# Kernel tuning notes

Measured on AMD Instinct MI355X. Metric: run time of the kernel, lower is better.

The kernel has to match this reference:

```python
import jax, jax.numpy as jnp
import numpy as np

E = 8        # num_experts
H = 2048     # hidden_size
I = 1408     # intermediate_size
K = 2        # top_k
B, S = 1, 2048


def setup_inputs() -> dict:
    key = jax.random.key(0)
    k1, k2, k3, k4, k5 = jax.random.split(key, 5)
    hidden_states = jax.random.normal(k1, (B, S, H), dtype=jnp.float32)
    top_k_index = jax.random.randint(k2, (B, S, K), 0, E, dtype=jnp.int32)
    top_k_weights = jax.random.uniform(k3, (B, S, K), dtype=jnp.float32)
    # scaled init so activations stay O(1)
    gate_up_proj = jax.random.normal(k4, (E, 2 * I, H), dtype=jnp.float32) / np.sqrt(H)
    down_proj = jax.random.normal(k5, (E, H, I), dtype=jnp.float32) / np.sqrt(I)
    return {
        "hidden_states": hidden_states,
        "top_k_index": top_k_index,
        "top_k_weights": top_k_weights,
        "gate_up_proj": gate_up_proj,
        "down_proj": down_proj,
    }


def reference(hidden_states, top_k_index, top_k_weights, gate_up_proj, down_proj):
    orig_shape = hidden_states.shape
    x = hidden_states.reshape(-1, H)            # [T, H]
    idx = top_k_index.reshape(-1, K)            # [T, K] int32
    w = top_k_weights.reshape(-1, K)            # [T, K]
    out = jnp.zeros_like(x)
    for e in range(E):
        # combine weight for tokens routed to expert e (0 if not routed)
        we = jnp.sum(w * (idx == e).astype(w.dtype), axis=-1)   # [T]
        gu = x @ gate_up_proj[e].T                              # [T, 2I]
        gate, up = gu[:, :I], gu[:, I:]
        h = jax.nn.silu(gate) * up                              # [T, I]
        y = h @ down_proj[e].T                                  # [T, H]
        out = out + we[:, None] * y
    return out.reshape(orig_shape)
```

## Files before the change

### kernel.cpp

```cpp
#include <hip/hip_runtime.h>
#include <hip/hip_bf16.h>

#define E_ 8
#define H_ 2048
#define I_ 1408
#define S_ 2048
#define NPAIR 4096
#define MAXMT 32

typedef short bf16x8 __attribute__((ext_vector_type(8)));
typedef ushort u16x8 __attribute__((ext_vector_type(8)));
typedef float f32x4  __attribute__((ext_vector_type(4)));

__device__ inline bf16x8 pack8(float4 a, float4 b) {
    bf16x8 r;
    const float v[8] = {a.x, a.y, a.z, a.w, b.x, b.y, b.z, b.w};
#pragma unroll
    for (int j = 0; j < 8; ++j) {
        __hip_bfloat16 t = __float2bfloat16(v[j]);
        r[j] = *reinterpret_cast<short*>(&t);
    }
    return r;
}

__global__ void moe_router(const int* __restrict__ idx,
                           int* __restrict__ counts, int* __restrict__ bases,
                           int* __restrict__ tok, int* __restrict__ inv) {
    __shared__ int cnt[E_];
    __shared__ int cur[E_];
    const int tid = threadIdx.x;
    if (tid < E_) cnt[tid] = 0;
    __syncthreads();
    for (int p = tid; p < NPAIR; p += 256)
        atomicAdd(&cnt[idx[p]], 1);
    __syncthreads();
    if (tid == 0) {
        int b = 0;
        for (int e = 0; e < E_; ++e) {
            counts[e] = cnt[e];
            bases[e]  = b;
            cur[e]    = b;
            b += cnt[e];
        }
    }
    __syncthreads();
    for (int p = tid; p < NPAIR; p += 256) {
        const int e = idx[p];
        const int pos = atomicAdd(&cur[e], 1);
        tok[pos] = p >> 1;
        inv[p]   = pos;
    }
}

__global__ void convert_x(const float* __restrict__ x, ushort* __restrict__ xb) {
    const size_t i = ((size_t)blockIdx.x * 256 + threadIdx.x) * 8;
    const float4 a = *(const float4*)(x + i);
    const float4 b = *(const float4*)(x + i + 4);
    *(bf16x8*)(xb + i) = pack8(a, b);
}

__global__ __launch_bounds__(256, 2)
void moe_gemm1(const ushort* __restrict__ xb,
               const float* __restrict__ wg,
               const int* __restrict__ counts,
               const int* __restrict__ bases,
               const int* __restrict__ tok,
               ushort* __restrict__ hbuf) {
    const int e  = blockIdx.y & (E_ - 1);
    const int mt = blockIdx.y >> 3;
    const int count = counts[e];
    if (mt * 128 >= count) return;
    const int base = bases[e];
    const int n0 = blockIdx.x * 128;
    const float* wge = wg + (size_t)e * (2 * I_) * H_;

    __shared__ alignas(16) ushort sm[2][3][5120];

    const int tid  = threadIdx.x;
    const int lane = tid & 63;
    const int wid  = tid >> 6;
    const int wm = wid & 1, wn = wid >> 1;
    const int lr = lane & 15, lq = lane >> 4;

    const f32x4 vzero = {0.f, 0.f, 0.f, 0.f};
    f32x4 accg[4][4], accu[4][4];
#pragma unroll
    for (int mi = 0; mi < 4; ++mi)
#pragma unroll
        for (int ni = 0; ni < 4; ++ni) { accg[mi][ni] = vzero; accu[mi][ni] = vzero; }

    const int srow = tid >> 2;
    const int sc8  = (tid & 3) * 8;
    const int r0 = srow, r1 = srow + 64;

    const int ia0 = mt * 128 + r0, ia1 = mt * 128 + r1;
    const bool v0 = ia0 < count, v1 = ia1 < count;
    const ushort* ap0 = xb + (size_t)(v0 ? tok[base + ia0] : 0) * H_ + sc8;
    const ushort* ap1 = xb + (size_t)(v1 ? tok[base + ia1] : 0) * H_ + sc8;
    const float* gp0 = wge + (size_t)(n0 + r0) * H_ + sc8;
    const float* gp1 = wge + (size_t)(n0 + r1) * H_ + sc8;
    const float* up0 = gp0 + (size_t)I_ * H_;
    const float* up1 = gp1 + (size_t)I_ * H_;

    const uint4 z4 = {0u, 0u, 0u, 0u};
    uint4 ra0, ra1;
    float4 rg0a, rg0b, rg1a, rg1b, ru0a, ru0b, ru1a, ru1b;

    ra0 = v0 ? *(const uint4*)ap0 : z4;
    ra1 = v1 ? *(const uint4*)ap1 : z4;
    rg0a = *(const float4*)gp0; rg0b = *(const float4*)(gp0 + 4);
    rg1a = *(const float4*)gp1; rg1b = *(const float4*)(gp1 + 4);
    ru0a = *(const float4*)up0; ru0b = *(const float4*)(up0 + 4);
    ru1a = *(const float4*)up1; ru1b = *(const float4*)(up1 + 4);
    {
        ushort* As = &sm[0][0][0]; ushort* Bg = &sm[0][1][0]; ushort* Bu = &sm[0][2][0];
        *(uint4*)&As[r0 * 40 + sc8] = ra0;
        *(uint4*)&As[r1 * 40 + sc8] = ra1;
        *(bf16x8*)&Bg[r0 * 40 + sc8] = pack8(rg0a, rg0b);
        *(bf16x8*)&Bg[r1 * 40 + sc8] = pack8(rg1a, rg1b);
        *(bf16x8*)&Bu[r0 * 40 + sc8] = pack8(ru0a, ru0b);
        *(bf16x8*)&Bu[r1 * 40 + sc8] = pack8(ru1a, ru1b);
    }
    __syncthreads();

    for (int kt = 0; kt < H_ / 32; ++kt) {
        const int cur = kt & 1;
        if (kt < H_ / 32 - 1) {
            ap0 += 32; ap1 += 32; gp0 += 32; gp1 += 32; up0 += 32; up1 += 32;
            ra0 = v0 ? *(const uint4*)ap0 : z4;
            ra1 = v1 ? *(const uint4*)ap1 : z4;
            rg0a = *(const float4*)gp0; rg0b = *(const float4*)(gp0 + 4);
            rg1a = *(const float4*)gp1; rg1b = *(const float4*)(gp1 + 4);
            ru0a = *(const float4*)up0; ru0b = *(const float4*)(up0 + 4);
            ru1a = *(const float4*)up1; ru1b = *(const float4*)(up1 + 4);
        }
        const ushort* As = &sm[cur][0][0];
        const ushort* Bg = &sm[cur][1][0];
        const ushort* Bu = &sm[cur][2][0];
        bf16x8 a[4], bg[4], bu[4];
#pragma unroll
        for (int mi = 0; mi < 4; ++mi)
            a[mi] = *(const bf16x8*)&As[(wm * 64 + mi * 16 + lr) * 40 + lq * 8];
#pragma unroll
        for (int ni = 0; ni < 4; ++ni) {
            bg[ni] = *(const bf16x8*)&Bg[(wn * 64 + ni * 16 + lr) * 40 + lq * 8];
            bu[ni] = *(const bf16x8*)&Bu[(wn * 64 + ni * 16 + lr) * 40 + lq * 8];
        }
#pragma unroll
        for (int mi = 0; mi < 4; ++mi)
#pragma unroll
            for (int ni = 0; ni < 4; ++ni) {
                accg[mi][ni] = __builtin_amdgcn_mfma_f32_16x16x32_bf16(a[mi], bg[ni], accg[mi][ni], 0, 0, 0);
                accu[mi][ni] = __builtin_amdgcn_mfma_f32_16x16x32_bf16(a[mi], bu[ni], accu[mi][ni], 0, 0, 0);
            }
        if (kt < H_ / 32 - 1) {
            ushort* nA = &sm[cur ^ 1][0][0];
            ushort* nG = &sm[cur ^ 1][1][0];
            ushort* nU = &sm[cur ^ 1][2][0];
            *(uint4*)&nA[r0 * 40 + sc8] = ra0;
            *(uint4*)&nA[r1 * 40 + sc8] = ra1;
            *(bf16x8*)&nG[r0 * 40 + sc8] = pack8(rg0a, rg0b);
            *(bf16x8*)&nG[r1 * 40 + sc8] = pack8(rg1a, rg1b);
            *(bf16x8*)&nU[r0 * 40 + sc8] = pack8(ru0a, ru0b);
            *(bf16x8*)&nU[r1 * 40 + sc8] = pack8(ru1a, ru1b);
        }
        __syncthreads();
    }

    ushort* Ht = &sm[0][0][0];
#pragma unroll
    for (int mi = 0; mi < 4; ++mi)
#pragma unroll
        for (int r = 0; r < 4; ++r) {
            const int row = wm * 64 + mi * 16 + lq * 4 + r;
#pragma unroll
            for (int ni = 0; ni < 4; ++ni) {
                const int col = wn * 64 + ni * 16 + lr;
                const float g = accg[mi][ni][r];
                const float u = accu[mi][ni][r];
                const float h = (g / (1.0f + __expf(-g))) * u;
                __hip_bfloat16 hb = __float2bfloat16(h);
                Ht[row * 136 + col] = *reinterpret_cast<ushort*>(&hb);
            }
        }
    __syncthreads();
#pragma unroll
    for (int p = 0; p < 8; ++p) {
        const int slot = p * 256 + tid;
        const int row = slot >> 4;
        const int cc  = (slot & 15) * 8;
        const int gi = mt * 128 + row;
        if (gi < count)
            *(uint4*)&hbuf[(size_t)(base + gi) * I_ + n0 + cc] = *(const uint4*)&Ht[row * 136 + cc];
    }
}

__global__ __launch_bounds__(256, 2)
void moe_gemm2(const ushort* __restrict__ hbuf,
               const float* __restrict__ wd,
               const int* __restrict__ counts,
               const int* __restrict__ bases,
               ushort* __restrict__ ybuf) {
    const int e  = blockIdx.y & (E_ - 1);
    const int mt = blockIdx.y >> 3;
    const int count = counts[e];
    if (mt * 128 >= count) return;
    const int base = bases[e];
    const int n0 = blockIdx.x * 128;
    const float* wde = wd + (size_t)e * H_ * I_;

    __shared__ alignas(16) ushort sm[2][2][5120];

    const int tid  = threadIdx.x;
    const int lane = tid & 63;
    const int wid  = tid >> 6;
    const int wm = wid & 1, wn = wid >> 1;
    const int lr = lane & 15, lq = lane >> 4;

    const f32x4 vzero = {0.f, 0.f, 0.f, 0.f};
    f32x4 acc[4][4];
#pragma unroll
    for (int mi = 0; mi < 4; ++mi)
#pragma unroll
        for (int ni = 0; ni < 4; ++ni) acc[mi][ni] = vzero;

    const int srow = tid >> 2;
    const int sc8  = (tid & 3) * 8;
    const int r0 = srow, r1 = srow + 64;

    const int ia0 = mt * 128 + r0, ia1 = mt * 128 + r1;
    const bool v0 = ia0 < count, v1 = ia1 < count;
    const ushort* ap0 = hbuf + (size_t)(base + (v0 ? ia0 : 0)) * I_ + sc8;
    const ushort* ap1 = hbuf + (size_t)(base + (v1 ? ia1 : 0)) * I_ + sc8;
    const float* bp0 = wde + (size_t)(n0 + r0) * I_ + sc8;
    const float* bp1 = wde + (size_t)(n0 + r1) * I_ + sc8;

    const uint4 z4 = {0u, 0u, 0u, 0u};
    uint4 ra0, ra1;
    float4 rb0a, rb0b, rb1a, rb1b;

    ra0 = v0 ? *(const uint4*)ap0 : z4;
    ra1 = v1 ? *(const uint4*)ap1 : z4;
    rb0a = *(const float4*)bp0; rb0b = *(const float4*)(bp0 + 4);
    rb1a = *(const float4*)bp1; rb1b = *(const float4*)(bp1 + 4);
    {
        ushort* As = &sm[0][0][0]; ushort* Bs = &sm[0][1][0];
        *(uint4*)&As[r0 * 40 + sc8] = ra0;
        *(uint4*)&As[r1 * 40 + sc8] = ra1;
        *(bf16x8*)&Bs[r0 * 40 + sc8] = pack8(rb0a, rb0b);
        *(bf16x8*)&Bs[r1 * 40 + sc8] = pack8(rb1a, rb1b);
    }
    __syncthreads();

    for (int kt = 0; kt < I_ / 32; ++kt) {
        const int cur = kt & 1;
        if (kt < I_ / 32 - 1) {
            ap0 += 32; ap1 += 32; bp0 += 32; bp1 += 32;
            ra0 = v0 ? *(const uint4*)ap0 : z4;
            ra1 = v1 ? *(const uint4*)ap1 : z4;
            rb0a = *(const float4*)bp0; rb0b = *(const float4*)(bp0 + 4);
            rb1a = *(const float4*)bp1; rb1b = *(const float4*)(bp1 + 4);
        }
        const ushort* As = &sm[cur][0][0];
        const ushort* Bs = &sm[cur][1][0];
        bf16x8 a[4], b[4];
#pragma unroll
        for (int mi = 0; mi < 4; ++mi)
            a[mi] = *(const bf16x8*)&As[(wm * 64 + mi * 16 + lr) * 40 + lq * 8];
#pragma unroll
        for (int ni = 0; ni < 4; ++ni)
            b[ni] = *(const bf16x8*)&Bs[(wn * 64 + ni * 16 + lr) * 40 + lq * 8];
#pragma unroll
        for (int mi = 0; mi < 4; ++mi)
#pragma unroll
            for (int ni = 0; ni < 4; ++ni)
                acc[mi][ni] = __builtin_amdgcn_mfma_f32_16x16x32_bf16(a[mi], b[ni], acc[mi][ni], 0, 0, 0);
        if (kt < I_ / 32 - 1) {
            ushort* nA = &sm[cur ^ 1][0][0];
            ushort* nB = &sm[cur ^ 1][1][0];
            *(uint4*)&nA[r0 * 40 + sc8] = ra0;
            *(uint4*)&nA[r1 * 40 + sc8] = ra1;
            *(bf16x8*)&nB[r0 * 40 + sc8] = pack8(rb0a, rb0b);
            *(bf16x8*)&nB[r1 * 40 + sc8] = pack8(rb1a, rb1b);
        }
        __syncthreads();
    }

    ushort* Yt = &sm[0][0][0];
#pragma unroll
    for (int mi = 0; mi < 4; ++mi)
#pragma unroll
        for (int r = 0; r < 4; ++r) {
            const int row = wm * 64 + mi * 16 + lq * 4 + r;
#pragma unroll
            for (int ni = 0; ni < 4; ++ni) {
                const int col = wn * 64 + ni * 16 + lr;
                __hip_bfloat16 yb = __float2bfloat16(acc[mi][ni][r]);
                Yt[row * 136 + col] = *reinterpret_cast<ushort*>(&yb);
            }
        }
    __syncthreads();
#pragma unroll
    for (int p = 0; p < 8; ++p) {
        const int slot = p * 256 + tid;
        const int row = slot >> 4;
        const int cc  = (slot & 15) * 8;
        const int gi = mt * 128 + row;
        if (gi < count)
            *(uint4*)&ybuf[(size_t)(base + gi) * H_ + n0 + cc] = *(const uint4*)&Yt[row * 136 + cc];
    }
}

__global__ void moe_combine(const ushort* __restrict__ ybuf,
                            const int* __restrict__ inv,
                            const float* __restrict__ tkw,
                            float* __restrict__ out) {
    const int t = blockIdx.x;
    const int c8 = threadIdx.x * 8;
    const int p0 = inv[2 * t], p1 = inv[2 * t + 1];
    const float w0 = tkw[2 * t], w1 = tkw[2 * t + 1];
    const u16x8 y0 = *(const u16x8*)(ybuf + (size_t)p0 * H_ + c8);
    const u16x8 y1 = *(const u16x8*)(ybuf + (size_t)p1 * H_ + c8);
    float o[8];
#pragma unroll
    for (int j = 0; j < 8; ++j) {
        const unsigned f0 = ((unsigned)y0[j]) << 16;
        const unsigned f1 = ((unsigned)y1[j]) << 16;
        o[j] = w0 * __uint_as_float(f0) + w1 * __uint_as_float(f1);
    }
    float* dst = out + (size_t)t * H_ + c8;
    *(float4*)dst       = make_float4(o[0], o[1], o[2], o[3]);
    *(float4*)(dst + 4) = make_float4(o[4], o[5], o[6], o[7]);
}

extern "C" void kernel_launch(void* const* d_in, const int* in_sizes, int n_in,
                              void* d_out, int out_size, void* d_ws, size_t ws_size,
                              hipStream_t stream) {
    const float* x   = (const float*)d_in[0];
    const int*   tki = (const int*)d_in[1];
    const float* tkw = (const float*)d_in[2];
    const float* wg  = (const float*)d_in[3];
    const float* wd  = (const float*)d_in[4];
    float* out = (float*)d_out;

    char* p = (char*)d_ws;
    int* counts = (int*)p;  p += 32;
    int* bases  = (int*)p;  p += 32;
    int* tok    = (int*)p;  p += NPAIR * sizeof(int);
    int* inv    = (int*)p;  p += NPAIR * sizeof(int);
    ushort* xb   = (ushort*)p; p += (size_t)S_ * H_ * 2;
    ushort* hbuf = (ushort*)p; p += (size_t)NPAIR * I_ * 2;
    ushort* ybuf = (ushort*)p; p += (size_t)NPAIR * H_ * 2;

    convert_x<<<dim3((S_ * H_) / (256 * 8)), 256, 0, stream>>>(x, xb);
    moe_router<<<dim3(1), 256, 0, stream>>>(tki, counts, bases, tok, inv);
    moe_gemm1<<<dim3(I_ / 128, E_ * MAXMT), 256, 0, stream>>>(xb, wg, counts, bases, tok, hbuf);
    moe_gemm2<<<dim3(H_ / 128, E_ * MAXMT), 256, 0, stream>>>(hbuf, wd, counts, bases, ybuf);
    moe_combine<<<dim3(S_), 256, 0, stream>>>(ybuf, inv, tkw, out);
}
```

Baseline: 427.9 us.

## Pre-convert weights to tiled bf16 and stream tiles with direct-to-LDS loads

Adds a kernel that converts both fp32 weight tensors each call into bf16 laid out as contiguous 128x32 tiles. The grouped GEMMs then load A and B tiles with global_load_lds straight into shared memory, replacing in-kernel fp32 loads and conversion. This removes repeated per-block fp32 weight conversion and halves the weight bytes read inside the GEMMs. In exchange it adds a full extra pass over all weights each call (fp32 read plus bf16 write, about 138 MB of fp32 plus 69 MB of bf16) and single-buffered loads with two barriers per k-step. The old fp32 GEMM kernels are kept as a fallback for when the workspace is too small.

```diff
diff --git a/kernel.cpp b/kernel.cpp
--- a/kernel.cpp
+++ b/kernel.cpp
@@ -8,6 +8,11 @@
 #define NPAIR 4096
 #define MAXMT 32
 
+#define NT1 22
+#define KT1 64
+#define NT2 16
+#define KT2 44
+
 typedef short bf16x8 __attribute__((ext_vector_type(8)));
 typedef ushort u16x8 __attribute__((ext_vector_type(8)));
 typedef float f32x4  __attribute__((ext_vector_type(4)));
@@ -21,6 +26,13 @@
         r[j] = *reinterpret_cast<short*>(&t);
     }
     return r;
+}
+
+__device__ __forceinline__ void gload16(const ushort* g, ushort* l) {
+    __builtin_amdgcn_global_load_lds(
+        (const __attribute__((address_space(1))) void*)g,
+        (__attribute__((address_space(3))) void*)l,
+        16, 0, 0);
 }
 
 __global__ void moe_router(const int* __restrict__ idx,
@@ -59,13 +71,240 @@
     *(bf16x8*)(xb + i) = pack8(a, b);
 }
 
+__global__ __launch_bounds__(256)
+void convert_w(const float* __restrict__ wg, const float* __restrict__ wd,
+               ushort* __restrict__ wgt, ushort* __restrict__ wdt) {
+    const int b = blockIdx.x;
+    const int tid = threadIdx.x;
+    const float* src;
+    ushort* dst;
+    int rowstride;
+    if (b < E_ * NT1 * KT1) {
+        const int e = b / (NT1 * KT1), rem = b % (NT1 * KT1);
+        const int nt = rem / KT1, kt = rem % KT1;
+        src = wg + ((size_t)e * (2 * I_) + nt * 128) * H_ + kt * 32;
+        dst = wgt + (size_t)b * 4096;
+        rowstride = H_;
+    } else {
+        const int b2 = b - E_ * NT1 * KT1;
+        const int e = b2 / (NT2 * KT2), rem = b2 % (NT2 * KT2);
+        const int nt = rem / KT2, kt = rem % KT2;
+        src = wd + ((size_t)e * H_ + nt * 128) * I_ + kt * 32;
+        dst = wdt + (size_t)b2 * 4096;
+        rowstride = I_;
+    }
+#pragma unroll
+    for (int i = 0; i < 2; ++i) {
+        const int c = tid + i * 256;
+        const int row = c >> 2, col = (c & 3) * 8;
+        const float* s = src + (size_t)row * rowstride + col;
+        const float4 a = *(const float4*)s;
+        const float4 bq = *(const float4*)(s + 4);
+        *(bf16x8*)(dst + c * 8) = pack8(a, bq);
+    }
+}
+
 __global__ __launch_bounds__(256, 2)
 void moe_gemm1(const ushort* __restrict__ xb,
-               const float* __restrict__ wg,
+               const ushort* __restrict__ wgt,
                const int* __restrict__ counts,
                const int* __restrict__ bases,
                const int* __restrict__ tok,
                ushort* __restrict__ hbuf) {
+    const int e  = blockIdx.y & (E_ - 1);
+    const int mt = blockIdx.y >> 3;
+    const int count = counts[e];
+    if (mt * 128 >= count) return;
+    const int base = bases[e];
+    const int nt = blockIdx.x;
+    const int n0 = nt * 128;
+
+    __shared__ alignas(16) ushort sm[17408];
+    ushort* smA = sm;
+    ushort* smG = sm + 4096;
+    ushort* smU = sm + 8192;
+
+    const int tid  = threadIdx.x;
+    const int lane = tid & 63;
+    const int wid  = tid >> 6;
+    const int wm = wid & 1, wn = wid >> 1;
+    const int lr = lane & 15, lq = lane >> 4;
+
+    const f32x4 vzero = {0.f, 0.f, 0.f, 0.f};
+    f32x4 accg[4][4], accu[4][4];
+#pragma unroll
+    for (int mi = 0; mi < 4; ++mi)
+#pragma unroll
+        for (int ni = 0; ni < 4; ++ni) { accg[mi][ni] = vzero; accu[mi][ni] = vzero; }
+
+    const int srow = tid >> 2;
+    const int sc8  = (tid & 3) * 8;
+    const int ia0 = mt * 128 + srow, ia1 = ia0 + 64;
+    const ushort* ap0 = xb + (size_t)(ia0 < count ? tok[base + ia0] : 0) * H_ + sc8;
+    const ushort* ap1 = xb + (size_t)(ia1 < count ? tok[base + ia1] : 0) * H_ + sc8;
+    const ushort* gp  = wgt + (size_t)(e * NT1 + nt) * KT1 * 4096 + tid * 8;
+    const ushort* up  = wgt + (size_t)(e * NT1 + nt + 11) * KT1 * 4096 + tid * 8;
+    ushort* dA0 = smA + tid * 8;
+    ushort* dA1 = smA + tid * 8 + 2048;
+    ushort* dG0 = smG + tid * 8;
+    ushort* dG1 = smG + tid * 8 + 2048;
+    ushort* dU0 = smU + tid * 8;
+    ushort* dU1 = smU + tid * 8 + 2048;
+
+    for (int kt = 0; kt < KT1; ++kt) {
+        gload16(ap0, dA0);
+        gload16(ap1, dA1);
+        gload16(gp,        dG0);
+        gload16(gp + 2048, dG1);
+        gload16(up,        dU0);
+        gload16(up + 2048, dU1);
+        ap0 += 32; ap1 += 32; gp += 4096; up += 4096;
+        __syncthreads();
+
+        bf16x8 a[4], bg[4], bu[4];
+#pragma unroll
+        for (int mi = 0; mi < 4; ++mi)
+            a[mi] = *(const bf16x8*)&smA[(wm * 64 + mi * 16 + lr) * 32 + lq * 8];
+#pragma unroll
+        for (int ni = 0; ni < 4; ++ni) {
+            bg[ni] = *(const bf16x8*)&smG[(wn * 64 + ni * 16 + lr) * 32 + lq * 8];
+            bu[ni] = *(const bf16x8*)&smU[(wn * 64 + ni * 16 + lr) * 32 + lq * 8];
+        }
+#pragma unroll
+        for (int mi = 0; mi < 4; ++mi)
+#pragma unroll
+            for (int ni = 0; ni < 4; ++ni) {
+                accg[mi][ni] = __builtin_amdgcn_mfma_f32_16x16x32_bf16(a[mi], bg[ni], accg[mi][ni], 0, 0, 0);
+                accu[mi][ni] = __builtin_amdgcn_mfma_f32_16x16x32_bf16(a[mi], bu[ni], accu[mi][ni], 0, 0, 0);
+            }
+        __syncthreads();
+    }
+
+    ushort* Ht = sm;
+#pragma unroll
+    for (int mi = 0; mi < 4; ++mi)
+#pragma unroll
+        for (int r = 0; r < 4; ++r) {
+            const int row = wm * 64 + mi * 16 + lq * 4 + r;
+#pragma unroll
+            for (int ni = 0; ni < 4; ++ni) {
+                const int col = wn * 64 + ni * 16 + lr;
+                const float g = accg[mi][ni][r];
+                const float u = accu[mi][ni][r];
+                const float h = (g / (1.0f + __expf(-g))) * u;
+                __hip_bfloat16 hb = __float2bfloat16(h);
+                Ht[row * 136 + col] = *reinterpret_cast<ushort*>(&hb);
+            }
+        }
+    __syncthreads();
+#pragma unroll
+    for (int p = 0; p < 8; ++p) {
+        const int slot = p * 256 + tid;
+        const int row = slot >> 4;
+        const int cc  = (slot & 15) * 8;
+        const int gi = mt * 128 + row;
+        if (gi < count)
+            *(uint4*)&hbuf[(size_t)(base + gi) * I_ + n0 + cc] = *(const uint4*)&Ht[row * 136 + cc];
+    }
+}
+
+__global__ __launch_bounds__(256, 2)
+void moe_gemm2(const ushort* __restrict__ hbuf,
+               const ushort* __restrict__ wdt,
+               const int* __restrict__ counts,
+               const int* __restrict__ bases,
+               ushort* __restrict__ ybuf) {
+    const int e  = blockIdx.y & (E_ - 1);
+    const int mt = blockIdx.y >> 3;
+    const int count = counts[e];
+    if (mt * 128 >= count) return;
+    const int base = bases[e];
+    const int nt = blockIdx.x;
+    const int n0 = nt * 128;
+
+    __shared__ alignas(16) ushort sm[17408];
+    ushort* smA = sm;
+    ushort* smB = sm + 4096;
+
+    const int tid  = threadIdx.x;
+    const int lane = tid & 63;
+    const int wid  = tid >> 6;
+    const int wm = wid & 1, wn = wid >> 1;
+    const int lr = lane & 15, lq = lane >> 4;
+
+    const f32x4 vzero = {0.f, 0.f, 0.f, 0.f};
+    f32x4 acc[4][4];
+#pragma unroll
+    for (int mi = 0; mi < 4; ++mi)
+#pragma unroll
+        for (int ni = 0; ni < 4; ++ni) acc[mi][ni] = vzero;
+
+    const int srow = tid >> 2;
+    const int sc8  = (tid & 3) * 8;
+    const int ia0 = mt * 128 + srow, ia1 = ia0 + 64;
+    const ushort* ap0 = hbuf + (size_t)(base + (ia0 < count ? ia0 : 0)) * I_ + sc8;
+    const ushort* ap1 = hbuf + (size_t)(base + (ia1 < count ? ia1 : 0)) * I_ + sc8;
+    const ushort* bp  = wdt + (size_t)(e * NT2 + nt) * KT2 * 4096 + tid * 8;
+    ushort* dA0 = smA + tid * 8;
+    ushort* dA1 = smA + tid * 8 + 2048;
+    ushort* dB0 = smB + tid * 8;
+    ushort* dB1 = smB + tid * 8 + 2048;
+
+    for (int kt = 0; kt < KT2; ++kt) {
+        gload16(ap0, dA0);
+        gload16(ap1, dA1);
+        gload16(bp,        dB0);
+        gload16(bp + 2048, dB1);
+        ap0 += 32; ap1 += 32; bp += 4096;
+        __syncthreads();
+
+        bf16x8 a[4], b[4];
+#pragma unroll
+        for (int mi = 0; mi < 4; ++mi)
+            a[mi] = *(const bf16x8*)&smA[(wm * 64 + mi * 16 + lr) * 32 + lq * 8];
+#pragma unroll
+        for (int ni = 0; ni < 4; ++ni)
+            b[ni] = *(const bf16x8*)&smB[(wn * 64 + ni * 16 + lr) * 32 + lq * 8];
+#pragma unroll
+        for (int mi = 0; mi < 4; ++mi)
+#pragma unroll
+            for (int ni = 0; ni < 4; ++ni)
+                acc[mi][ni] = __builtin_amdgcn_mfma_f32_16x16x32_bf16(a[mi], b[ni], acc[mi][ni], 0, 0, 0);
+        __syncthreads();
+    }
+
+    ushort* Yt = sm;
+#pragma unroll
+    for (int mi = 0; mi < 4; ++mi)
+#pragma unroll
+        for (int r = 0; r < 4; ++r) {
+            const int row = wm * 64 + mi * 16 + lq * 4 + r;
+#pragma unroll
+            for (int ni = 0; ni < 4; ++ni) {
+                const int col = wn * 64 + ni * 16 + lr;
+                __hip_bfloat16 yb = __float2bfloat16(acc[mi][ni][r]);
+                Yt[row * 136 + col] = *reinterpret_cast<ushort*>(&yb);
+            }
+        }
+    __syncthreads();
+#pragma unroll
+    for (int p = 0; p < 8; ++p) {
+        const int slot = p * 256 + tid;
+        const int row = slot >> 4;
+        const int cc  = (slot & 15) * 8;
+        const int gi = mt * 128 + row;
+        if (gi < count)
+            *(uint4*)&ybuf[(size_t)(base + gi) * H_ + n0 + cc] = *(const uint4*)&Yt[row * 136 + cc];
+    }
+}
+
+__global__ __launch_bounds__(256, 2)
+void moe_gemm1_f32(const ushort* __restrict__ xb,
+                   const float* __restrict__ wg,
+                   const int* __restrict__ counts,
+                   const int* __restrict__ bases,
+                   const int* __restrict__ tok,
+                   ushort* __restrict__ hbuf) {
     const int e  = blockIdx.y & (E_ - 1);
     const int mt = blockIdx.y >> 3;
     const int count = counts[e];
@@ -196,11 +435,11 @@
 }
 
 __global__ __launch_bounds__(256, 2)
-void moe_gemm2(const ushort* __restrict__ hbuf,
-               const float* __restrict__ wd,
-               const int* __restrict__ counts,
-               const int* __restrict__ bases,
-               ushort* __restrict__ ybuf) {
+void moe_gemm2_f32(const ushort* __restrict__ hbuf,
+                   const float* __restrict__ wd,
+                   const int* __restrict__ counts,
+                   const int* __restrict__ bases,
+                   ushort* __restrict__ ybuf) {
     const int e  = blockIdx.y & (E_ - 1);
     const int mt = blockIdx.y >> 3;
     const int count = counts[e];
@@ -351,10 +590,20 @@
     ushort* xb   = (ushort*)p; p += (size_t)S_ * H_ * 2;
     ushort* hbuf = (ushort*)p; p += (size_t)NPAIR * I_ * 2;
     ushort* ybuf = (ushort*)p; p += (size_t)NPAIR * H_ * 2;
+    ushort* wgt  = (ushort*)p; p += (size_t)E_ * (2 * I_) * H_ * 2;
+    ushort* wdt  = (ushort*)p; p += (size_t)E_ * H_ * I_ * 2;
+    const size_t need = (size_t)(p - (char*)d_ws);
 
     convert_x<<<dim3((S_ * H_) / (256 * 8)), 256, 0, stream>>>(x, xb);
     moe_router<<<dim3(1), 256, 0, stream>>>(tki, counts, bases, tok, inv);
-    moe_gemm1<<<dim3(I_ / 128, E_ * MAXMT), 256, 0, stream>>>(xb, wg, counts, bases, tok, hbuf);
-    moe_gemm2<<<dim3(H_ / 128, E_ * MAXMT), 256, 0, stream>>>(hbuf, wd, counts, bases, ybuf);
+
+    if (ws_size >= need) {
+        convert_w<<<dim3(E_ * NT1 * KT1 + E_ * NT2 * KT2), 256, 0, stream>>>(wg, wd, wgt, wdt);
+        moe_gemm1<<<dim3(I_ / 128, E_ * MAXMT), 256, 0, stream>>>(xb, wgt, counts, bases, tok, hbuf);
+        moe_gemm2<<<dim3(H_ / 128, E_ * MAXMT), 256, 0, stream>>>(hbuf, wdt, counts, bases, ybuf);
+    } else {
+        moe_gemm1_f32<<<dim3(I_ / 128, E_ * MAXMT), 256, 0, stream>>>(xb, wg, counts, bases, tok, hbuf);
+        moe_gemm2_f32<<<dim3(H_ / 128, E_ * MAXMT), 256, 0, stream>>>(hbuf, wd, counts, bases, ybuf);
+    }
     moe_combine<<<dim3(S_), 256, 0, stream>>>(ybuf, inv, tkw, out);
 }
```

After: 493.4 us. 15.3% more time.

## Pre-convert weights to bf16 and stream GEMM tiles via direct global-to-LDS loads

Applied to the files above, without the earlier changes.

Adds a single conversion kernel that casts all expert weights and x to bf16 and also does the routing, replacing the separate convert_x and router launches. The GEMMs then read bf16 weights with global_load_lds asynchronous copies into an unpadded LDS double buffer, using manual vmcnt waits and barriers. This removes the per-tile fp32 weight loads and in-register packing in the GEMM inner loops, which were re-done by every token tile. The cost is an extra full pass that reads the fp32 weights and writes bf16 copies on every call. LDS rows also lose their padding, which may cause bank conflicts.

```diff
diff --git a/kernel.cpp b/kernel.cpp
--- a/kernel.cpp
+++ b/kernel.cpp
@@ -8,6 +8,13 @@
 #define NPAIR 4096
 #define MAXMT 32
 
+#define KT1 64
+#define KT2 44
+
+#define WGBLK 22528
+#define WDBLK 11264
+#define XBLK   2048
+
 typedef short bf16x8 __attribute__((ext_vector_type(8)));
 typedef ushort u16x8 __attribute__((ext_vector_type(8)));
 typedef float f32x4  __attribute__((ext_vector_type(4)));
@@ -23,45 +30,63 @@
     return r;
 }
 
-__global__ void moe_router(const int* __restrict__ idx,
-                           int* __restrict__ counts, int* __restrict__ bases,
-                           int* __restrict__ tok, int* __restrict__ inv) {
+__device__ __forceinline__ void gload16(const ushort* g, ushort* l) {
+    __builtin_amdgcn_global_load_lds(
+        (const __attribute__((address_space(1))) void*)g,
+        (__attribute__((address_space(3))) void*)l,
+        16, 0, 0);
+}
+
+__global__ __launch_bounds__(256)
+void convert_all(const float* __restrict__ wg, const float* __restrict__ wd,
+                 const float* __restrict__ x, const int* __restrict__ tki,
+                 ushort* __restrict__ wgb, ushort* __restrict__ wdb,
+                 ushort* __restrict__ xb,
+                 int* __restrict__ counts, int* __restrict__ bases,
+                 int* __restrict__ tok, int* __restrict__ inv) {
+    const int b = blockIdx.x;
+    const int tid = threadIdx.x;
+    if (b < WGBLK + WDBLK + XBLK) {
+        const float* src;
+        ushort* dst;
+        size_t off;
+        if (b < WGBLK)              { src = wg; dst = wgb; off = (size_t)b * 2048; }
+        else if (b < WGBLK + WDBLK) { src = wd; dst = wdb; off = (size_t)(b - WGBLK) * 2048; }
+        else                        { src = x;  dst = xb;  off = (size_t)(b - WGBLK - WDBLK) * 2048; }
+        const size_t i = off + (size_t)tid * 8;
+        const float4 a = *(const float4*)(src + i);
+        const float4 c = *(const float4*)(src + i + 4);
+        *(bf16x8*)(dst + i) = pack8(a, c);
+        return;
+    }
     __shared__ int cnt[E_];
     __shared__ int cur[E_];
-    const int tid = threadIdx.x;
     if (tid < E_) cnt[tid] = 0;
     __syncthreads();
     for (int p = tid; p < NPAIR; p += 256)
-        atomicAdd(&cnt[idx[p]], 1);
+        atomicAdd(&cnt[tki[p]], 1);
     __syncthreads();
     if (tid == 0) {
-        int b = 0;
+        int bb = 0;
         for (int e = 0; e < E_; ++e) {
             counts[e] = cnt[e];
-            bases[e]  = b;
-            cur[e]    = b;
-            b += cnt[e];
+            bases[e]  = bb;
+            cur[e]    = bb;
+            bb += cnt[e];
         }
     }
     __syncthreads();
     for (int p = tid; p < NPAIR; p += 256) {
-        const int e = idx[p];
+        const int e = tki[p];
         const int pos = atomicAdd(&cur[e], 1);
         tok[pos] = p >> 1;
         inv[p]   = pos;
     }
 }
 
-__global__ void convert_x(const float* __restrict__ x, ushort* __restrict__ xb) {
-    const size_t i = ((size_t)blockIdx.x * 256 + threadIdx.x) * 8;
-    const float4 a = *(const float4*)(x + i);
-    const float4 b = *(const float4*)(x + i + 4);
-    *(bf16x8*)(xb + i) = pack8(a, b);
-}
-
 __global__ __launch_bounds__(256, 2)
 void moe_gemm1(const ushort* __restrict__ xb,
-               const float* __restrict__ wg,
+               const ushort* __restrict__ wgb,
                const int* __restrict__ counts,
                const int* __restrict__ bases,
                const int* __restrict__ tok,
@@ -71,10 +96,11 @@
     const int count = counts[e];
     if (mt * 128 >= count) return;
     const int base = bases[e];
-    const int n0 = blockIdx.x * 128;
-    const float* wge = wg + (size_t)e * (2 * I_) * H_;
-
-    __shared__ alignas(16) ushort sm[2][3][5120];
+    const int nt = blockIdx.x;
+    const int n0 = nt * 128;
+    const ushort* wgbe = wgb + (size_t)e * (2 * I_) * H_;
+
+    __shared__ alignas(16) ushort sm[24576];
 
     const int tid  = threadIdx.x;
     const int lane = tid & 63;
@@ -91,60 +117,49 @@
 
     const int srow = tid >> 2;
     const int sc8  = (tid & 3) * 8;
-    const int r0 = srow, r1 = srow + 64;
-
-    const int ia0 = mt * 128 + r0, ia1 = mt * 128 + r1;
-    const bool v0 = ia0 < count, v1 = ia1 < count;
-    const ushort* ap0 = xb + (size_t)(v0 ? tok[base + ia0] : 0) * H_ + sc8;
-    const ushort* ap1 = xb + (size_t)(v1 ? tok[base + ia1] : 0) * H_ + sc8;
-    const float* gp0 = wge + (size_t)(n0 + r0) * H_ + sc8;
-    const float* gp1 = wge + (size_t)(n0 + r1) * H_ + sc8;
-    const float* up0 = gp0 + (size_t)I_ * H_;
-    const float* up1 = gp1 + (size_t)I_ * H_;
-
-    const uint4 z4 = {0u, 0u, 0u, 0u};
-    uint4 ra0, ra1;
-    float4 rg0a, rg0b, rg1a, rg1b, ru0a, ru0b, ru1a, ru1b;
-
-    ra0 = v0 ? *(const uint4*)ap0 : z4;
-    ra1 = v1 ? *(const uint4*)ap1 : z4;
-    rg0a = *(const float4*)gp0; rg0b = *(const float4*)(gp0 + 4);
-    rg1a = *(const float4*)gp1; rg1b = *(const float4*)(gp1 + 4);
-    ru0a = *(const float4*)up0; ru0b = *(const float4*)(up0 + 4);
-    ru1a = *(const float4*)up1; ru1b = *(const float4*)(up1 + 4);
+    const int ia0 = mt * 128 + srow, ia1 = ia0 + 64;
+    const ushort* ap0 = xb + (size_t)(ia0 < count ? tok[base + ia0] : 0) * H_ + sc8;
+    const ushort* ap1 = xb + (size_t)(ia1 < count ? tok[base + ia1] : 0) * H_ + sc8;
+    const ushort* gp0 = wgbe + (size_t)(n0 + srow) * H_ + sc8;
+    const ushort* gp1 = gp0 + (size_t)64 * H_;
+    const ushort* up0 = wgbe + (size_t)(I_ + n0 + srow) * H_ + sc8;
+    const ushort* up1 = up0 + (size_t)64 * H_;
+
+    const int d0 = tid * 8, d1 = tid * 8 + 2048;
+
     {
-        ushort* As = &sm[0][0][0]; ushort* Bg = &sm[0][1][0]; ushort* Bu = &sm[0][2][0];
-        *(uint4*)&As[r0 * 40 + sc8] = ra0;
-        *(uint4*)&As[r1 * 40 + sc8] = ra1;
-        *(bf16x8*)&Bg[r0 * 40 + sc8] = pack8(rg0a, rg0b);
-        *(bf16x8*)&Bg[r1 * 40 + sc8] = pack8(rg1a, rg1b);
-        *(bf16x8*)&Bu[r0 * 40 + sc8] = pack8(ru0a, ru0b);
-        *(bf16x8*)&Bu[r1 * 40 + sc8] = pack8(ru1a, ru1b);
-    }
-    __syncthreads();
-
-    for (int kt = 0; kt < H_ / 32; ++kt) {
-        const int cur = kt & 1;
-        if (kt < H_ / 32 - 1) {
+        ushort* bA = sm; ushort* bG = sm + 4096; ushort* bU = sm + 8192;
+        gload16(ap0, bA + d0); gload16(ap1, bA + d1);
+        gload16(gp0, bG + d0); gload16(gp1, bG + d1);
+        gload16(up0, bU + d0); gload16(up1, bU + d1);
+    }
+
+    for (int kt = 0; kt < KT1; ++kt) {
+        ushort* curb = sm + (kt & 1) * 12288;
+        if (kt + 1 < KT1) {
             ap0 += 32; ap1 += 32; gp0 += 32; gp1 += 32; up0 += 32; up1 += 32;
-            ra0 = v0 ? *(const uint4*)ap0 : z4;
-            ra1 = v1 ? *(const uint4*)ap1 : z4;
-            rg0a = *(const float4*)gp0; rg0b = *(const float4*)(gp0 + 4);
-            rg1a = *(const float4*)gp1; rg1b = *(const float4*)(gp1 + 4);
-            ru0a = *(const float4*)up0; ru0b = *(const float4*)(up0 + 4);
-            ru1a = *(const float4*)up1; ru1b = *(const float4*)(up1 + 4);
-        }
-        const ushort* As = &sm[cur][0][0];
-        const ushort* Bg = &sm[cur][1][0];
-        const ushort* Bu = &sm[cur][2][0];
+            ushort* nb = sm + ((kt + 1) & 1) * 12288;
+            gload16(ap0, nb + d0);        gload16(ap1, nb + d1);
+            gload16(gp0, nb + 4096 + d0); gload16(gp1, nb + 4096 + d1);
+            gload16(up0, nb + 8192 + d0); gload16(up1, nb + 8192 + d1);
+            asm volatile("s_waitcnt vmcnt(6)" ::: "memory");
+        } else {
+            asm volatile("s_waitcnt vmcnt(0)" ::: "memory");
+        }
+        __builtin_amdgcn_s_barrier();
+        __builtin_amdgcn_sched_barrier(0);
+
+        const ushort* As = curb;
+        const ushort* Bg = curb + 4096;
+        const ushort* Bu = curb + 8192;
         bf16x8 a[4], bg[4], bu[4];
 #pragma unroll
         for (int mi = 0; mi < 4; ++mi)
-            a[mi] = *(const bf16x8*)&As[(wm * 64 + mi * 16 + lr) * 40 + lq * 8];
+            a[mi] = *(const bf16x8*)&As[(wm * 64 + mi * 16 + lr) * 32 + lq * 8];
 #pragma unroll
         for (int ni = 0; ni < 4; ++ni) {
-            bg[ni] = *(const bf16x8*)&Bg[(wn * 64 + ni * 16 + lr) * 40 + lq * 8];
-            bu[ni] = *(const bf16x8*)&Bu[(wn * 64 + ni * 16 + lr) * 40 + lq * 8];
+            bg[ni] = *(const bf16x8*)&Bg[(wn * 64 + ni * 16 + lr) * 32 + lq * 8];
+            bu[ni] = *(const bf16x8*)&Bu[(wn * 64 + ni * 16 + lr) * 32 + lq * 8];
         }
 #pragma unroll
         for (int mi = 0; mi < 4; ++mi)
@@ -153,21 +168,11 @@
                 accg[mi][ni] = __builtin_amdgcn_mfma_f32_16x16x32_bf16(a[mi], bg[ni], accg[mi][ni], 0, 0, 0);
                 accu[mi][ni] = __builtin_amdgcn_mfma_f32_16x16x32_bf16(a[mi], bu[ni], accu[mi][ni], 0, 0, 0);
             }
-        if (kt < H_ / 32 - 1) {
-            ushort* nA = &sm[cur ^ 1][0][0];
-            ushort* nG = &sm[cur ^ 1][1][0];
-            ushort* nU = &sm[cur ^ 1][2][0];
-            *(uint4*)&nA[r0 * 40 + sc8] = ra0;
-            *(uint4*)&nA[r1 * 40 + sc8] = ra1;
-            *(bf16x8*)&nG[r0 * 40 + sc8] = pack8(rg0a, rg0b);
-            *(bf16x8*)&nG[r1 * 40 + sc8] = pack8(rg1a, rg1b);
-            *(bf16x8*)&nU[r0 * 40 + sc8] = pack8(ru0a, ru0b);
-            *(bf16x8*)&nU[r1 * 40 + sc8] = pack8(ru1a, ru1b);
-        }
-        __syncthreads();
-    }
-
-    ushort* Ht = &sm[0][0][0];
+        __builtin_amdgcn_sched_barrier(0);
+        __builtin_amdgcn_s_barrier();
+    }
+
+    ushort* Ht = sm;
 #pragma unroll
     for (int mi = 0; mi < 4; ++mi)
 #pragma unroll
@@ -197,7 +202,7 @@
 
 __global__ __launch_bounds__(256, 2)
 void moe_gemm2(const ushort* __restrict__ hbuf,
-               const float* __restrict__ wd,
+               const ushort* __restrict__ wdb,
                const int* __restrict__ counts,
                const int* __restrict__ bases,
                ushort* __restrict__ ybuf) {
@@ -206,10 +211,11 @@
     const int count = counts[e];
     if (mt * 128 >= count) return;
     const int base = bases[e];
-    const int n0 = blockIdx.x * 128;
-    const float* wde = wd + (size_t)e * H_ * I_;
-
-    __shared__ alignas(16) ushort sm[2][2][5120];
+    const int nt = blockIdx.x;
+    const int n0 = nt * 128;
+    const ushort* wdbe = wdb + (size_t)e * H_ * I_;
+
+    __shared__ alignas(16) ushort sm[17408];
 
     const int tid  = threadIdx.x;
     const int lane = tid & 63;
@@ -226,67 +232,53 @@
 
     const int srow = tid >> 2;
     const int sc8  = (tid & 3) * 8;
-    const int r0 = srow, r1 = srow + 64;
-
-    const int ia0 = mt * 128 + r0, ia1 = mt * 128 + r1;
-    const bool v0 = ia0 < count, v1 = ia1 < count;
-    const ushort* ap0 = hbuf + (size_t)(base + (v0 ? ia0 : 0)) * I_ + sc8;
-    const ushort* ap1 = hbuf + (size_t)(base + (v1 ? ia1 : 0)) * I_ + sc8;
-    const float* bp0 = wde + (size_t)(n0 + r0) * I_ + sc8;
-    const float* bp1 = wde + (size_t)(n0 + r1) * I_ + sc8;
-
-    const uint4 z4 = {0u, 0u, 0u, 0u};
-    uint4 ra0, ra1;
-    float4 rb0a, rb0b, rb1a, rb1b;
-
-    ra0 = v0 ? *(const uint4*)ap0 : z4;
-    ra1 = v1 ? *(const uint4*)ap1 : z4;
-    rb0a = *(const float4*)bp0; rb0b = *(const float4*)(bp0 + 4);
-    rb1a = *(const float4*)bp1; rb1b = *(const float4*)(bp1 + 4);
+    const int ia0 = mt * 128 + srow, ia1 = ia0 + 64;
+    const ushort* ap0 = hbuf + (size_t)(base + (ia0 < count ? ia0 : 0)) * I_ + sc8;
+    const ushort* ap1 = hbuf + (size_t)(base + (ia1 < count ? ia1 : 0)) * I_ + sc8;
+    const ushort* bp0 = wdbe + (size_t)(n0 + srow) * I_ + sc8;
+    const ushort* bp1 = bp0 + (size_t)64 * I_;
+
+    const int d0 = tid * 8, d1 = tid * 8 + 2048;
+
     {
-        ushort* As = &sm[0][0][0]; ushort* Bs = &sm[0][1][0];
-        *(uint4*)&As[r0 * 40 + sc8] = ra0;
-        *(uint4*)&As[r1 * 40 + sc8] = ra1;
-        *(bf16x8*)&Bs[r0 * 40 + sc8] = pack8(rb0a, rb0b);
-        *(bf16x8*)&Bs[r1 * 40 + sc8] = pack8(rb1a, rb1b);
-    }
-    __syncthreads();
-
-    for (int kt = 0; kt < I_ / 32; ++kt) {
-        const int cur = kt & 1;
-        if (kt < I_ / 32 - 1) {
+        ushort* bA = sm; ushort* bB = sm + 4096;
+        gload16(ap0, bA + d0); gload16(ap1, bA + d1);
+        gload16(bp0, bB + d0); gload16(bp1, bB + d1);
+    }
+
+    for (int kt = 0; kt < KT2; ++kt) {
+        ushort* curb = sm + (kt & 1) * 8192;
+        if (kt + 1 < KT2) {
             ap0 += 32; ap1 += 32; bp0 += 32; bp1 += 32;
-            ra0 = v0 ? *(const uint4*)ap0 : z4;
-            ra1 = v1 ? *(const uint4*)ap1 : z4;
-            rb0a = *(const float4*)bp0; rb0b = *(const float4*)(bp0 + 4);
-            rb1a = *(const float4*)bp1; rb1b = *(const float4*)(bp1 + 4);
-        }
-        const ushort* As = &sm[cur][0][0];
-        const ushort* Bs = &sm[cur][1][0];
+            ushort* nb = sm + ((kt + 1) & 1) * 8192;
+            gload16(ap0, nb + d0);        gload16(ap1, nb + d1);
+            gload16(bp0, nb + 4096 + d0); gload16(bp1, nb + 4096 + d1);
+            asm volatile("s_waitcnt vmcnt(4)" ::: "memory");
+        } else {
+            asm volatile("s_waitcnt vmcnt(0)" ::: "memory");
+        }
+        __builtin_amdgcn_s_barrier();
+        __builtin_amdgcn_sched_barrier(0);
+
+        const ushort* As = curb;
+        const ushort* Bs = curb + 4096;
         bf16x8 a[4], b[4];
 #pragma unroll
         for (int mi = 0; mi < 4; ++mi)
-            a[mi] = *(const bf16x8*)&As[(wm * 64 + mi * 16 + lr) * 40 + lq * 8];
+            a[mi] = *(const bf16x8*)&As[(wm * 64 + mi * 16 + lr) * 32 + lq * 8];
 #pragma unroll
         for (int ni = 0; ni < 4; ++ni)
-            b[ni] = *(const bf16x8*)&Bs[(wn * 64 + ni * 16 + lr) * 40 + lq * 8];
+            b[ni] = *(const bf16x8*)&Bs[(wn * 64 + ni * 16 + lr) * 32 + lq * 8];
 #pragma unroll
         for (int mi = 0; mi < 4; ++mi)
 #pragma unroll
             for (int ni = 0; ni < 4; ++ni)
                 acc[mi][ni] = __builtin_amdgcn_mfma_f32_16x16x32_bf16(a[mi], b[ni], acc[mi][ni], 0, 0, 0);
-        if (kt < I_ / 32 - 1) {
-            ushort* nA = &sm[cur ^ 1][0][0];
-            ushort* nB = &sm[cur ^ 1][1][0];
-            *(uint4*)&nA[r0 * 40 + sc8] = ra0;
-            *(uint4*)&nA[r1 * 40 + sc8] = ra1;
-            *(bf16x8*)&nB[r0 * 40 + sc8] = pack8(rb0a, rb0b);
-            *(bf16x8*)&nB[r1 * 40 + sc8] = pack8(rb1a, rb1b);
-        }
-        __syncthreads();
-    }
-
-    ushort* Yt = &sm[0][0][0];
+        __builtin_amdgcn_sched_barrier(0);
+        __builtin_amdgcn_s_barrier();
+    }
+
+    ushort* Yt = sm;
 #pragma unroll
     for (int mi = 0; mi < 4; ++mi)
 #pragma unroll
@@ -351,10 +343,12 @@
     ushort* xb   = (ushort*)p; p += (size_t)S_ * H_ * 2;
     ushort* hbuf = (ushort*)p; p += (size_t)NPAIR * I_ * 2;
     ushort* ybuf = (ushort*)p; p += (size_t)NPAIR * H_ * 2;
-
-    convert_x<<<dim3((S_ * H_) / (256 * 8)), 256, 0, stream>>>(x, xb);
-    moe_router<<<dim3(1), 256, 0, stream>>>(tki, counts, bases, tok, inv);
-    moe_gemm1<<<dim3(I_ / 128, E_ * MAXMT), 256, 0, stream>>>(xb, wg, counts, bases, tok, hbuf);
-    moe_gemm2<<<dim3(H_ / 128, E_ * MAXMT), 256, 0, stream>>>(hbuf, wd, counts, bases, ybuf);
+    ushort* wgb  = (ushort*)p; p += (size_t)E_ * (2 * I_) * H_ * 2;
+    ushort* wdb  = (ushort*)p; p += (size_t)E_ * H_ * I_ * 2;
+
+    convert_all<<<dim3(WGBLK + WDBLK + XBLK + 1), 256, 0, stream>>>(
+        wg, wd, x, tki, wgb, wdb, xb, counts, bases, tok, inv);
+    moe_gemm1<<<dim3(I_ / 128, E_ * MAXMT), 256, 0, stream>>>(xb, wgb, counts, bases, tok, hbuf);
+    moe_gemm2<<<dim3(H_ / 128, E_ * MAXMT), 256, 0, stream>>>(hbuf, wdb, counts, bases, ybuf);
     moe_combine<<<dim3(S_), 256, 0, stream>>>(ybuf, inv, tkw, out);
 }
```

New measurement: 474.0 us. +10.8%, slower.
